# Optimization experiments

Hardware: AMD Instinct MI355X
Metric: run time of the kernel (lower is better)

Reference implementation:

```python
import jax, jax.numpy as jnp
import numpy as np

N_NODES = 100000
N_EDGES = 1600000
D = 128
L = 4          # GIN layers
H = 32         # inner MLP hidden width (hard-coded in create_mlp)
BN_EPS = 1e-5


def setup_inputs() -> dict:
    key = jax.random.key(0)
    ks = jax.random.split(key, 8)
    X = jax.random.normal(ks[0], (N_NODES, D), dtype=jnp.float32)
    edge_index = jax.random.randint(ks[1], (2, N_EDGES), 0, N_NODES, dtype=jnp.int64)
    eps = jax.random.normal(ks[2], (L,), dtype=jnp.float32)
    W1 = jax.random.normal(ks[3], (L, H, D), dtype=jnp.float32) * 0.1
    W2 = jax.random.normal(ks[4], (L, H, H), dtype=jnp.float32) * 0.1
    W3 = jax.random.normal(ks[5], (L, D, H), dtype=jnp.float32) * 0.1
    return {
        "X": X, "edge_index": edge_index, "eps": eps,
        "W1": W1, "b1": jnp.zeros((L, H), jnp.float32),
        "g1": jnp.ones((L, H), jnp.float32), "bt1": jnp.zeros((L, H), jnp.float32),
        "W2": W2, "b2": jnp.zeros((L, H), jnp.float32),
        "g2": jnp.ones((L, H), jnp.float32), "bt2": jnp.zeros((L, H), jnp.float32),
        "W3": W3, "b3": jnp.zeros((L, D), jnp.float32),
    }


def _bn(x, g, b):
    # BatchNorm1d in training mode: biased batch stats over the node axis
    m = jnp.mean(x, axis=0)
    v = jnp.var(x, axis=0)
    return g * (x - m) * jax.lax.rsqrt(v + BN_EPS) + b


def reference(X, edge_index, eps, W1, b1, g1, bt1, W2, b2, g2, bt2, W3, b3):
    src, dst = edge_index[0], edge_index[1]
    for l in range(L):
        # identity-message scatter-add neighbor aggregation
        S = jax.ops.segment_sum(X[src], dst, num_segments=N_NODES)  # [N, D_l]
        Z = (1.0 + eps[l]) * X + S
        # inner MLP: Lin->BN->ReLU, Lin->BN->ReLU, Lin
        h = jax.nn.relu(_bn(Z @ W1[l].T + b1[l], g1[l], bt1[l]))
        h = jax.nn.relu(_bn(h @ W2[l].T + b2[l], g2[l], bt2[l]))
        X = h @ W3[l].T + b3[l]
    return X
```

## Files before the change

kernel.cpp:

```cpp
#include <hip/hip_runtime.h>

#define NN 100000
#define NE 1600000
#define DD 128
#define HH 32
#define NB 196
#define SB 256
#define EPB 6250
#define BCAP 12288
#define QS 25000

#define OFF_P        0UL
#define OFF_T        12800000UL
#define OFF_PK       25600000UL
#define OFF_QOFF     32000000UL
#define OFF_COUNTS   33600128UL
#define OFF_POFS     33800832UL
#define OFF_BTOT     34001536UL
#define OFF_BBASE    34002560UL
#define OFF_STATS    34003584UL
#define OFF_W1T      34019968UL
#define OFF_W2T      34036352UL
#define OFF_MT       34052736UL
#define OFF_C        34065024UL
#define OFF_W3T      34065536UL

__device__ __forceinline__ int src_quad(int s) {
    return (s >= 2 * QS) ? ((s >= 3 * QS) ? 3 : 2) : ((s >= QS) ? 1 : 0);
}

__global__ void __launch_bounds__(256) k_init(const int* __restrict__ ei,
                                              int* __restrict__ counts,
                                              const float* __restrict__ W1,
                                              const float* __restrict__ W2,
                                              const float* __restrict__ W3,
                                              const float* __restrict__ b3,
                                              float* __restrict__ W1T,
                                              float* __restrict__ W2T,
                                              float* __restrict__ MT,
                                              float* __restrict__ C,
                                              float* __restrict__ W3T) {
    int t = threadIdx.x;
    if (blockIdx.x < SB) {
        __shared__ int c[NB];
        if (t < NB) c[t] = 0;
        __syncthreads();
        int s = blockIdx.x * EPB;
        for (int e = s + t; e < s + EPB; e += 256)
            atomicAdd(&c[ei[NE + e] >> 9], 1);
        __syncthreads();
        if (t < NB) counts[t * SB + blockIdx.x] = c[t];
        return;
    }
    int b = blockIdx.x - SB;
    if (b < 12) {
        int d = b * 256 + t;
        int l = d >> 10, rem = d & 1023;
        int i = rem >> 5, j = rem & 31;
        const float* w1r = W1 + (l + 1) * HH * DD + i * DD;
        const float* w3c = W3 + l * DD * HH + j;
        float m = 0.f;
#pragma unroll 8
        for (int k = 0; k < DD; k++) m += w1r[k] * w3c[k * HH];
        MT[l * 1024 + j * 32 + i] = m;
    } else if (b == 12) {
        for (int idx = t; idx < 4096; idx += 256) {
            int jj = idx >> 7, kk = idx & 127;
            W1T[kk * 32 + jj] = W1[jj * 128 + kk];
        }
    } else if (b == 13) {
        for (int idx = t; idx < 4096; idx += 256) {
            int l = idx >> 10, rem = idx & 1023;
            int i = rem >> 5, j = rem & 31;
            W2T[l * 1024 + j * 32 + i] = W2[l * 1024 + i * 32 + j];
        }
    } else if (b == 14) {
        for (int idx = t; idx < 4096; idx += 256) {
            int jj = idx >> 5, kk = idx & 31;
            W3T[kk * 128 + jj] = W3[3 * 4096 + jj * 32 + kk];
        }
    } else {
        if (t < 96) {
            int l = t >> 5, ii = t & 31;
            const float* w1r = W1 + (l + 1) * HH * DD + ii * DD;
            const float* bb = b3 + l * DD;
            float c = 0.f;
#pragma unroll 8
            for (int k = 0; k < DD; k++) c += w1r[k] * bb[k];
            C[l * 32 + ii] = c;
        }
    }
}

__global__ void __launch_bounds__(256) k_scanX(const int* __restrict__ counts,
                                               int* __restrict__ pofs,
                                               int* __restrict__ btot) {
    __shared__ int s[256];
    int t = threadIdx.x, b = blockIdx.x;
    int v = counts[b * SB + t];
    s[t] = v;
    __syncthreads();
    for (int off = 1; off < 256; off <<= 1) {
        int x = (t >= off) ? s[t - off] : 0;
        __syncthreads();
        s[t] += x;
        __syncthreads();
    }
    pofs[b * SB + t] = s[t] - v;
    if (t == 255) btot[b] = s[255];
}

__global__ void __launch_bounds__(256) k_scanY(const int* __restrict__ btot,
                                               int* __restrict__ bbase,
                                               int* __restrict__ qoff) {
    __shared__ int s[256];
    int t = threadIdx.x;
    int v = (t < NB) ? btot[t] : 0;
    s[t] = v;
    __syncthreads();
    for (int off = 1; off < 256; off <<= 1) {
        int x = (t >= off) ? s[t - off] : 0;
        __syncthreads();
        s[t] += x;
        __syncthreads();
    }
    if (t < NB) bbase[t] = s[t] - v;
    if (t == NB - 1) bbase[NB] = s[t];
    if (t == 0) qoff[4 * NN] = NE;
}

__global__ void __launch_bounds__(256) k_scatter(const int* __restrict__ ei,
                                                 const int* __restrict__ pofs,
                                                 const int* __restrict__ bbase,
                                                 int* __restrict__ pk) {
    __shared__ int cur[NB];
    int t = threadIdx.x, blk = blockIdx.x;
    if (t < NB) cur[t] = bbase[t] + pofs[t * SB + blk];
    __syncthreads();
    int s = blk * EPB;
    for (int e = s + t; e < s + EPB; e += 256) {
        int src = ei[e], dst = ei[NE + e];
        int b = dst >> 9;
        int pos = atomicAdd(&cur[b], 1);
        pk[pos] = (src << 9) | (dst & 511);
    }
}

__global__ void __launch_bounds__(256) k_bucket(int* pk,
                                                const int* __restrict__ bbase,
                                                int* __restrict__ qoff) {
    __shared__ int cnt[2048];
    __shared__ int ts[256];
    __shared__ int stage[BCAP];
    int t = threadIdx.x, b = blockIdx.x;
    int base = bbase[b], end = bbase[b + 1];
#pragma unroll
    for (int j = 0; j < 8; j++) cnt[t * 8 + j] = 0;
    __syncthreads();
    for (int e = base + t; e < end; e += 256) {
        int v = pk[e];
        atomicAdd(&cnt[((v & 511) << 2) | src_quad(v >> 9)], 1);
    }
    __syncthreads();
    int c8[8];
    int p = 0;
#pragma unroll
    for (int j = 0; j < 8; j++) { c8[j] = cnt[t * 8 + j]; p += c8[j]; }
    ts[t] = p;
    __syncthreads();
    for (int off = 1; off < 256; off <<= 1) {
        int x = (t >= off) ? ts[t - off] : 0;
        __syncthreads();
        ts[t] += x;
        __syncthreads();
    }
    int run = ts[t] - p;
#pragma unroll
    for (int j = 0; j < 8; j++) {
        int ci = t * 8 + j;
        cnt[ci] = run;
        int n0 = b * 512 + (ci >> 2);
        if (n0 < NN) qoff[n0 * 4 + (ci & 3)] = base + run;
        run += c8[j];
    }
    __syncthreads();
    for (int e = base + t; e < end; e += 256) {
        int v = pk[e];
        int src = v >> 9;
        int pos = atomicAdd(&cnt[((v & 511) << 2) | src_quad(src)], 1);
        stage[pos] = src;
    }
    __syncthreads();
    int sz = end - base;
    for (int i = t; i < sz; i += 256) pk[base + i] = stage[i];
}

__global__ void __launch_bounds__(256) k_P(const float4* __restrict__ X4,
                                           const float4* __restrict__ W1T4,
                                           float4* __restrict__ P4) {
    __shared__ float xs[128 * 33];
    int t = threadIdx.x, blk = blockIdx.x;
    int i = t & 7, g = t >> 3;
    int nbase = blk * 128;
    float4 acc[4];
#pragma unroll
    for (int j = 0; j < 4; j++) acc[j] = make_float4(0.f, 0.f, 0.f, 0.f);
    for (int kt = 0; kt < 4; kt++) {
        __syncthreads();
#pragma unroll
        for (int q = 0; q < 4; q++) {
            int idx = t + 256 * q;
            int nd = idx >> 3, c4 = idx & 7;
            int node = nbase + nd;
            if (node > NN - 1) node = NN - 1;
            float4 v = X4[(size_t)node * 32 + kt * 8 + c4];
            float* dst = xs + nd * 33 + 4 * c4;
            dst[0] = v.x; dst[1] = v.y; dst[2] = v.z; dst[3] = v.w;
        }
        __syncthreads();
        const float4* Wk = W1T4 + (size_t)(kt * 32) * 8 + i;
        const float* xr0 = xs + (g * 4) * 33;
#pragma unroll
        for (int k = 0; k < 32; k++) {
            float4 w = Wk[k * 8];
            float x0 = xr0[k], x1 = xr0[33 + k], x2 = xr0[66 + k], x3 = xr0[99 + k];
            acc[0].x += x0 * w.x; acc[0].y += x0 * w.y; acc[0].z += x0 * w.z; acc[0].w += x0 * w.w;
            acc[1].x += x1 * w.x; acc[1].y += x1 * w.y; acc[1].z += x1 * w.z; acc[1].w += x1 * w.w;
            acc[2].x += x2 * w.x; acc[2].y += x2 * w.y; acc[2].z += x2 * w.z; acc[2].w += x2 * w.w;
            acc[3].x += x3 * w.x; acc[3].y += x3 * w.y; acc[3].z += x3 * w.z; acc[3].w += x3 * w.w;
        }
    }
    int node = nbase + g * 4;
#pragma unroll
    for (int j = 0; j < 4; j++)
        if (node + j < NN) P4[(size_t)(node + j) * 8 + i] = acc[j];
}

__global__ void __launch_bounds__(256) k_A(const float4* __restrict__ P4,
                                           const int* __restrict__ csr,
                                           const int* __restrict__ qoff,
                                           const float* __restrict__ eps,
                                           const float* __restrict__ b1, int l,
                                           float4* __restrict__ T4,
                                           float* __restrict__ gs) {
    __shared__ float ls[64];
    int t = threadIdx.x;
    if (t < 64) ls[t] = 0.f;
    __syncthreads();
    int g = t >> 3, i = t & 7;
    int n = blockIdx.x * 32 + g;
    float e1 = 1.f + eps[l];
    int e0 = qoff[4 * n], eend = qoff[4 * n + 4];
    float4 p = P4[(size_t)n * 8 + i];
    float4 acc;
    acc.x = e1 * p.x; acc.y = e1 * p.y; acc.z = e1 * p.z; acc.w = e1 * p.w;
    int e = e0;
    for (; e + 8 <= eend; e += 8) {
        int s0 = csr[e], s1 = csr[e + 1], s2 = csr[e + 2], s3 = csr[e + 3];
        int s4 = csr[e + 4], s5 = csr[e + 5], s6 = csr[e + 6], s7 = csr[e + 7];
        float4 q0 = P4[(size_t)s0 * 8 + i];
        float4 q1 = P4[(size_t)s1 * 8 + i];
        float4 q2 = P4[(size_t)s2 * 8 + i];
        float4 q3 = P4[(size_t)s3 * 8 + i];
        float4 q4 = P4[(size_t)s4 * 8 + i];
        float4 q5 = P4[(size_t)s5 * 8 + i];
        float4 q6 = P4[(size_t)s6 * 8 + i];
        float4 q7 = P4[(size_t)s7 * 8 + i];
        acc.x += ((q0.x + q1.x) + (q2.x + q3.x)) + ((q4.x + q5.x) + (q6.x + q7.x));
        acc.y += ((q0.y + q1.y) + (q2.y + q3.y)) + ((q4.y + q5.y) + (q6.y + q7.y));
        acc.z += ((q0.z + q1.z) + (q2.z + q3.z)) + ((q4.z + q5.z) + (q6.z + q7.z));
        acc.w += ((q0.w + q1.w) + (q2.w + q3.w)) + ((q4.w + q5.w) + (q6.w + q7.w));
    }
    for (; e + 4 <= eend; e += 4) {
        int s0 = csr[e], s1 = csr[e + 1], s2 = csr[e + 2], s3 = csr[e + 3];
        float4 q0 = P4[(size_t)s0 * 8 + i];
        float4 q1 = P4[(size_t)s1 * 8 + i];
        float4 q2 = P4[(size_t)s2 * 8 + i];
        float4 q3 = P4[(size_t)s3 * 8 + i];
        acc.x += (q0.x + q1.x) + (q2.x + q3.x);
        acc.y += (q0.y + q1.y) + (q2.y + q3.y);
        acc.z += (q0.z + q1.z) + (q2.z + q3.z);
        acc.w += (q0.w + q1.w) + (q2.w + q3.w);
    }
    for (; e < eend; e++) {
        int s = csr[e];
        float4 q = P4[(size_t)s * 8 + i];
        acc.x += q.x; acc.y += q.y; acc.z += q.z; acc.w += q.w;
    }
    float4 bb = ((const float4*)(b1 + l * 32))[i];
    acc.x += bb.x; acc.y += bb.y; acc.z += bb.z; acc.w += bb.w;
    T4[(size_t)n * 8 + i] = acc;
    float sx = acc.x, sy = acc.y, sz = acc.z, sw = acc.w;
    float qx = acc.x * acc.x, qy = acc.y * acc.y, qz = acc.z * acc.z, qw = acc.w * acc.w;
#pragma unroll
    for (int off = 8; off < 64; off <<= 1) {
        sx += __shfl_xor(sx, off); sy += __shfl_xor(sy, off);
        sz += __shfl_xor(sz, off); sw += __shfl_xor(sw, off);
        qx += __shfl_xor(qx, off); qy += __shfl_xor(qy, off);
        qz += __shfl_xor(qz, off); qw += __shfl_xor(qw, off);
    }
    if ((t & 56) == 0) {
        atomicAdd(&ls[4 * i + 0], sx); atomicAdd(&ls[4 * i + 1], sy);
        atomicAdd(&ls[4 * i + 2], sz); atomicAdd(&ls[4 * i + 3], sw);
        atomicAdd(&ls[32 + 4 * i + 0], qx); atomicAdd(&ls[32 + 4 * i + 1], qy);
        atomicAdd(&ls[32 + 4 * i + 2], qz); atomicAdd(&ls[32 + 4 * i + 3], qw);
    }
    __syncthreads();
    if (t < 64) atomicAdd(&gs[(blockIdx.x & 7) * 64 + t], ls[t]);
}

__global__ void __launch_bounds__(256) k_D(float4* __restrict__ T4,
                                           const float4* __restrict__ W2T4,
                                           const float* __restrict__ b2,
                                           const float* __restrict__ g1,
                                           const float* __restrict__ bt1, int l,
                                           float* __restrict__ gs) {
    __shared__ float sc[32], sh[32], ls[64], a1s[128 * 33];
    int t = threadIdx.x, blk = blockIdx.x;
    if (t < 32) {
        float s0 = 0.f, s1 = 0.f;
#pragma unroll
        for (int r = 0; r < 8; r++) { s0 += gs[r * 64 + t]; s1 += gs[r * 64 + 32 + t]; }
        float m = s0 * (1.f / NN);
        float var = s1 * (1.f / NN) - m * m;
        float s = g1[l * 32 + t] * rsqrtf(var + 1e-5f);
        sc[t] = s; sh[t] = bt1[l * 32 + t] - m * s;
    } else if (t >= 64 && t < 128) {
        ls[t - 64] = 0.f;
    }
    __syncthreads();
    int nbase = blk * 128;
#pragma unroll
    for (int q = 0; q < 4; q++) {
        int idx = t + 256 * q;
        int nd = idx >> 3, c4 = idx & 7;
        int node = nbase + nd;
        if (node > NN - 1) node = NN - 1;
        float4 x = T4[(size_t)node * 8 + c4];
        float* dst = a1s + nd * 33 + 4 * c4;
        dst[0] = fmaxf(x.x * sc[4 * c4 + 0] + sh[4 * c4 + 0], 0.f);
        dst[1] = fmaxf(x.y * sc[4 * c4 + 1] + sh[4 * c4 + 1], 0.f);
        dst[2] = fmaxf(x.z * sc[4 * c4 + 2] + sh[4 * c4 + 2], 0.f);
        dst[3] = fmaxf(x.w * sc[4 * c4 + 3] + sh[4 * c4 + 3], 0.f);
    }
    __syncthreads();
    int i = t & 7, g = t >> 3;
    const float4* b24 = (const float4*)(b2 + l * 32);
    float4 b = b24[i];
    float4 acc[4];
#pragma unroll
    for (int j = 0; j < 4; j++) acc[j] = b;
    const float* xr0 = a1s + (g * 4) * 33;
#pragma unroll
    for (int k = 0; k < 32; k++) {
        float4 w = W2T4[k * 8 + i];
        float x0 = xr0[k], x1 = xr0[33 + k], x2 = xr0[66 + k], x3 = xr0[99 + k];
        acc[0].x += x0 * w.x; acc[0].y += x0 * w.y; acc[0].z += x0 * w.z; acc[0].w += x0 * w.w;
        acc[1].x += x1 * w.x; acc[1].y += x1 * w.y; acc[1].z += x1 * w.z; acc[1].w += x1 * w.w;
        acc[2].x += x2 * w.x; acc[2].y += x2 * w.y; acc[2].z += x2 * w.z; acc[2].w += x2 * w.w;
        acc[3].x += x3 * w.x; acc[3].y += x3 * w.y; acc[3].z += x3 * w.z; acc[3].w += x3 * w.w;
    }
    int node = nbase + g * 4;
    float sx = 0.f, sy = 0.f, sz = 0.f, sw = 0.f;
    float qx = 0.f, qy = 0.f, qz = 0.f, qw = 0.f;
#pragma unroll
    for (int j = 0; j < 4; j++) {
        if (node + j < NN) {
            T4[(size_t)(node + j) * 8 + i] = acc[j];
            sx += acc[j].x; sy += acc[j].y; sz += acc[j].z; sw += acc[j].w;
            qx += acc[j].x * acc[j].x; qy += acc[j].y * acc[j].y;
            qz += acc[j].z * acc[j].z; qw += acc[j].w * acc[j].w;
        }
    }
#pragma unroll
    for (int off = 8; off < 64; off <<= 1) {
        sx += __shfl_xor(sx, off); sy += __shfl_xor(sy, off);
        sz += __shfl_xor(sz, off); sw += __shfl_xor(sw, off);
        qx += __shfl_xor(qx, off); qy += __shfl_xor(qy, off);
        qz += __shfl_xor(qz, off); qw += __shfl_xor(qw, off);
    }
    if ((t & 56) == 0) {
        atomicAdd(&ls[4 * i + 0], sx); atomicAdd(&ls[4 * i + 1], sy);
        atomicAdd(&ls[4 * i + 2], sz); atomicAdd(&ls[4 * i + 3], sw);
        atomicAdd(&ls[32 + 4 * i + 0], qx); atomicAdd(&ls[32 + 4 * i + 1], qy);
        atomicAdd(&ls[32 + 4 * i + 2], qz); atomicAdd(&ls[32 + 4 * i + 3], qw);
    }
    __syncthreads();
    if (t < 64) atomicAdd(&gs[512 + (blk & 7) * 64 + t], ls[t]);
}

__global__ void __launch_bounds__(256) k_Fm(const float4* __restrict__ T4,
                                            const float* __restrict__ g2,
                                            const float* __restrict__ bt2, int l,
                                            const float* __restrict__ gs,
                                            const float4* __restrict__ MT4,
                                            const float* __restrict__ C,
                                            float4* __restrict__ P4) {
    __shared__ float sc[32], sh[32], a2s[128 * 33];
    int t = threadIdx.x, blk = blockIdx.x;
    if (t < 32) {
        float s0 = 0.f, s1 = 0.f;
#pragma unroll
        for (int r = 0; r < 8; r++) { s0 += gs[512 + r * 64 + t]; s1 += gs[512 + r * 64 + 32 + t]; }
        float m = s0 * (1.f / NN);
        float var = s1 * (1.f / NN) - m * m;
        float s = g2[l * 32 + t] * rsqrtf(var + 1e-5f);
        sc[t] = s; sh[t] = bt2[l * 32 + t] - m * s;
    }
    __syncthreads();
    int nbase = blk * 128;
#pragma unroll
    for (int q = 0; q < 4; q++) {
        int idx = t + 256 * q;
        int nd = idx >> 3, c4 = idx & 7;
        int node = nbase + nd;
        if (node > NN - 1) node = NN - 1;
        float4 x = T4[(size_t)node * 8 + c4];
        float* dst = a2s + nd * 33 + 4 * c4;
        dst[0] = fmaxf(x.x * sc[4 * c4 + 0] + sh[4 * c4 + 0], 0.f);
        dst[1] = fmaxf(x.y * sc[4 * c4 + 1] + sh[4 * c4 + 1], 0.f);
        dst[2] = fmaxf(x.z * sc[4 * c4 + 2] + sh[4 * c4 + 2], 0.f);
        dst[3] = fmaxf(x.w * sc[4 * c4 + 3] + sh[4 * c4 + 3], 0.f);
    }
    __syncthreads();
    int i = t & 7, g = t >> 3;
    const float4* C4 = (const float4*)(C + l * 32);
    float4 c0 = C4[i];
    float4 acc[4];
#pragma unroll
    for (int j = 0; j < 4; j++) acc[j] = c0;
    const float* xr0 = a2s + (g * 4) * 33;
    const float4* Mt = MT4 + l * 256;
#pragma unroll
    for (int k = 0; k < 32; k++) {
        float4 w = Mt[k * 8 + i];
        float x0 = xr0[k], x1 = xr0[33 + k], x2 = xr0[66 + k], x3 = xr0[99 + k];
        acc[0].x += x0 * w.x; acc[0].y += x0 * w.y; acc[0].z += x0 * w.z; acc[0].w += x0 * w.w;
        acc[1].x += x1 * w.x; acc[1].y += x1 * w.y; acc[1].z += x1 * w.z; acc[1].w += x1 * w.w;
        acc[2].x += x2 * w.x; acc[2].y += x2 * w.y; acc[2].z += x2 * w.z; acc[2].w += x2 * w.w;
        acc[3].x += x3 * w.x; acc[3].y += x3 * w.y; acc[3].z += x3 * w.z; acc[3].w += x3 * w.w;
    }
    int node = nbase + g * 4;
#pragma unroll
    for (int j = 0; j < 4; j++)
        if (node + j < NN) P4[(size_t)(node + j) * 8 + i] = acc[j];
}

__global__ void __launch_bounds__(256) k_F3(const float4* __restrict__ T4,
                                            const float* __restrict__ g2,
                                            const float* __restrict__ bt2,
                                            const float* __restrict__ gs,
                                            const float4* __restrict__ W3T4,
                                            const float* __restrict__ b3,
                                            float4* __restrict__ out4) {
    __shared__ float sc[32], sh[32], a2s[32 * 33];
    int t = threadIdx.x, blk = blockIdx.x;
    if (t < 32) {
        float s0 = 0.f, s1 = 0.f;
#pragma unroll
        for (int r = 0; r < 8; r++) { s0 += gs[512 + r * 64 + t]; s1 += gs[512 + r * 64 + 32 + t]; }
        float m = s0 * (1.f / NN);
        float var = s1 * (1.f / NN) - m * m;
        float s = g2[3 * 32 + t] * rsqrtf(var + 1e-5f);
        sc[t] = s; sh[t] = bt2[3 * 32 + t] - m * s;
    }
    __syncthreads();
    {
        int nd = t >> 3, c4 = t & 7;
        float4 x = T4[(size_t)(blk * 32 + nd) * 8 + c4];
        float* dst = a2s + nd * 33 + 4 * c4;
        dst[0] = fmaxf(x.x * sc[4 * c4 + 0] + sh[4 * c4 + 0], 0.f);
        dst[1] = fmaxf(x.y * sc[4 * c4 + 1] + sh[4 * c4 + 1], 0.f);
        dst[2] = fmaxf(x.z * sc[4 * c4 + 2] + sh[4 * c4 + 2], 0.f);
        dst[3] = fmaxf(x.w * sc[4 * c4 + 3] + sh[4 * c4 + 3], 0.f);
    }
    __syncthreads();
    int j = t & 31, g = t >> 5;
    const float4* b34 = (const float4*)(b3 + 3 * 128);
    float4 b = b34[j];
    float4 acc[4];
#pragma unroll
    for (int jj = 0; jj < 4; jj++) acc[jj] = b;
    const float* xr0 = a2s + (g * 4) * 33;
#pragma unroll
    for (int k = 0; k < 32; k++) {
        float4 w = W3T4[k * 32 + j];
        float x0 = xr0[k], x1 = xr0[33 + k], x2 = xr0[66 + k], x3 = xr0[99 + k];
        acc[0].x += x0 * w.x; acc[0].y += x0 * w.y; acc[0].z += x0 * w.z; acc[0].w += x0 * w.w;
        acc[1].x += x1 * w.x; acc[1].y += x1 * w.y; acc[1].z += x1 * w.z; acc[1].w += x1 * w.w;
        acc[2].x += x2 * w.x; acc[2].y += x2 * w.y; acc[2].z += x2 * w.z; acc[2].w += x2 * w.w;
        acc[3].x += x3 * w.x; acc[3].y += x3 * w.y; acc[3].z += x3 * w.z; acc[3].w += x3 * w.w;
    }
    size_t node = (size_t)blk * 32 + g * 4;
#pragma unroll
    for (int jj = 0; jj < 4; jj++)
        out4[(node + jj) * 32 + j] = acc[jj];
}

extern "C" void kernel_launch(void* const* d_in, const int* in_sizes, int n_in,
                              void* d_out, int out_size, void* d_ws, size_t ws_size,
                              hipStream_t stream) {
    const float* X   = (const float*)d_in[0];
    const int*   EI  = (const int*)d_in[1];
    const float* eps = (const float*)d_in[2];
    const float* W1  = (const float*)d_in[3];
    const float* b1  = (const float*)d_in[4];
    const float* g1  = (const float*)d_in[5];
    const float* bt1 = (const float*)d_in[6];
    const float* W2  = (const float*)d_in[7];
    const float* b2  = (const float*)d_in[8];
    const float* g2  = (const float*)d_in[9];
    const float* bt2 = (const float*)d_in[10];
    const float* W3  = (const float*)d_in[11];
    const float* b3  = (const float*)d_in[12];

    char* ws = (char*)d_ws;
    float* P       = (float*)(ws + OFF_P);
    float* T       = (float*)(ws + OFF_T);
    int*   pk      = (int*)(ws + OFF_PK);
    int*   qoff    = (int*)(ws + OFF_QOFF);
    int*   counts  = (int*)(ws + OFF_COUNTS);
    int*   pofs    = (int*)(ws + OFF_POFS);
    int*   btot    = (int*)(ws + OFF_BTOT);
    int*   bbase   = (int*)(ws + OFF_BBASE);
    float* stats   = (float*)(ws + OFF_STATS);
    float* W1T     = (float*)(ws + OFF_W1T);
    float* W2T     = (float*)(ws + OFF_W2T);
    float* MT      = (float*)(ws + OFF_MT);
    float* C       = (float*)(ws + OFF_C);
    float* W3T     = (float*)(ws + OFF_W3T);

    hipMemsetAsync(ws + OFF_STATS, 0, 16384, stream);

    k_init<<<SB + 16, 256, 0, stream>>>(EI, counts, W1, W2, W3, b3,
                                        W1T, W2T, MT, C, W3T);
    k_scanX<<<NB, 256, 0, stream>>>(counts, pofs, btot);
    k_scanY<<<1, 256, 0, stream>>>(btot, bbase, qoff);
    k_scatter<<<SB, 256, 0, stream>>>(EI, pofs, bbase, pk);
    k_bucket<<<NB, 256, 0, stream>>>(pk, bbase, qoff);
    k_P<<<782, 256, 0, stream>>>((const float4*)X, (const float4*)W1T, (float4*)P);

    for (int l = 0; l < 4; l++) {
        float* gs = stats + l * 1024;
        k_A<<<NN / 32, 256, 0, stream>>>((const float4*)P, pk, qoff, eps, b1, l,
                                         (float4*)T, gs);
        k_D<<<782, 256, 0, stream>>>((float4*)T,
                                     (const float4*)(W2T + (size_t)l * 1024),
                                     b2, g1, bt1, l, gs);
        if (l < 3)
            k_Fm<<<782, 256, 0, stream>>>((const float4*)T, g2, bt2, l, gs,
                                          (const float4*)MT, C, (float4*)P);
        else
            k_F3<<<3125, 256, 0, stream>>>((const float4*)T, g2, bt2, gs,
                                           (const float4*)W3T, b3, (float4*)d_out);
    }
}
```

Before: 462.8 us.

## Fuse preprocessing kernels: fold scans into scatter/bucket, merge P projection into init

Removes the two prefix-scan kernels and the stats memset by having each scatter and bucket block redundantly recompute bucket totals and offsets from the counts matrix. The first-layer projection (k_P) moves into the init launch as extra blocks, each transposing W1 into shared memory instead of reading a precomputed global W1T. The aim is fewer launches and dependency bubbles, at the cost of redundant per-block scans over 196x256 counts and larger shared memory in the init kernel.

```diff
diff --git a/kernel.cpp b/kernel.cpp
--- a/kernel.cpp
+++ b/kernel.cpp
@@ -15,11 +15,7 @@
 #define OFF_PK       25600000UL
 #define OFF_QOFF     32000000UL
 #define OFF_COUNTS   33600128UL
-#define OFF_POFS     33800832UL
-#define OFF_BTOT     34001536UL
-#define OFF_BBASE    34002560UL
 #define OFF_STATS    34003584UL
-#define OFF_W1T      34019968UL
 #define OFF_W2T      34036352UL
 #define OFF_MT       34052736UL
 #define OFF_C        34065024UL
@@ -35,21 +31,24 @@
                                               const float* __restrict__ W2,
                                               const float* __restrict__ W3,
                                               const float* __restrict__ b3,
-                                              float* __restrict__ W1T,
                                               float* __restrict__ W2T,
                                               float* __restrict__ MT,
                                               float* __restrict__ C,
-                                              float* __restrict__ W3T) {
+                                              float* __restrict__ W3T,
+                                              float* __restrict__ stats,
+                                              const float4* __restrict__ X4,
+                                              float4* __restrict__ P4) {
+    __shared__ __align__(16) char smem[33280];
     int t = threadIdx.x;
     if (blockIdx.x < SB) {
-        __shared__ int c[NB];
+        int* c = (int*)smem;
         if (t < NB) c[t] = 0;
         __syncthreads();
         int s = blockIdx.x * EPB;
         for (int e = s + t; e < s + EPB; e += 256)
             atomicAdd(&c[ei[NE + e] >> 9], 1);
         __syncthreads();
-        if (t < NB) counts[t * SB + blockIdx.x] = c[t];
+        if (t < NB) counts[blockIdx.x * 256 + t] = c[t];
         return;
     }
     int b = blockIdx.x - SB;
@@ -63,23 +62,21 @@
 #pragma unroll 8
         for (int k = 0; k < DD; k++) m += w1r[k] * w3c[k * HH];
         MT[l * 1024 + j * 32 + i] = m;
+        return;
     } else if (b == 12) {
-        for (int idx = t; idx < 4096; idx += 256) {
-            int jj = idx >> 7, kk = idx & 127;
-            W1T[kk * 32 + jj] = W1[jj * 128 + kk];
-        }
-    } else if (b == 13) {
         for (int idx = t; idx < 4096; idx += 256) {
             int l = idx >> 10, rem = idx & 1023;
             int i = rem >> 5, j = rem & 31;
             W2T[l * 1024 + j * 32 + i] = W2[l * 1024 + i * 32 + j];
         }
-    } else if (b == 14) {
+        return;
+    } else if (b == 13) {
         for (int idx = t; idx < 4096; idx += 256) {
             int jj = idx >> 5, kk = idx & 31;
             W3T[kk * 128 + jj] = W3[3 * 4096 + jj * 32 + kk];
         }
-    } else {
+        return;
+    } else if (b == 14) {
         if (t < 96) {
             int l = t >> 5, ii = t & 31;
             const float* w1r = W1 + (l + 1) * HH * DD + ii * DD;
@@ -89,117 +86,17 @@
             for (int k = 0; k < DD; k++) c += w1r[k] * bb[k];
             C[l * 32 + ii] = c;
         }
-    }
-}
-
-__global__ void __launch_bounds__(256) k_scanX(const int* __restrict__ counts,
-                                               int* __restrict__ pofs,
-                                               int* __restrict__ btot) {
-    __shared__ int s[256];
-    int t = threadIdx.x, b = blockIdx.x;
-    int v = counts[b * SB + t];
-    s[t] = v;
-    __syncthreads();
-    for (int off = 1; off < 256; off <<= 1) {
-        int x = (t >= off) ? s[t - off] : 0;
-        __syncthreads();
-        s[t] += x;
-        __syncthreads();
-    }
-    pofs[b * SB + t] = s[t] - v;
-    if (t == 255) btot[b] = s[255];
-}
-
-__global__ void __launch_bounds__(256) k_scanY(const int* __restrict__ btot,
-                                               int* __restrict__ bbase,
-                                               int* __restrict__ qoff) {
-    __shared__ int s[256];
-    int t = threadIdx.x;
-    int v = (t < NB) ? btot[t] : 0;
-    s[t] = v;
-    __syncthreads();
-    for (int off = 1; off < 256; off <<= 1) {
-        int x = (t >= off) ? s[t - off] : 0;
-        __syncthreads();
-        s[t] += x;
-        __syncthreads();
-    }
-    if (t < NB) bbase[t] = s[t] - v;
-    if (t == NB - 1) bbase[NB] = s[t];
-    if (t == 0) qoff[4 * NN] = NE;
-}
-
-__global__ void __launch_bounds__(256) k_scatter(const int* __restrict__ ei,
-                                                 const int* __restrict__ pofs,
-                                                 const int* __restrict__ bbase,
-                                                 int* __restrict__ pk) {
-    __shared__ int cur[NB];
-    int t = threadIdx.x, blk = blockIdx.x;
-    if (t < NB) cur[t] = bbase[t] + pofs[t * SB + blk];
-    __syncthreads();
-    int s = blk * EPB;
-    for (int e = s + t; e < s + EPB; e += 256) {
-        int src = ei[e], dst = ei[NE + e];
-        int b = dst >> 9;
-        int pos = atomicAdd(&cur[b], 1);
-        pk[pos] = (src << 9) | (dst & 511);
-    }
-}
-
-__global__ void __launch_bounds__(256) k_bucket(int* pk,
-                                                const int* __restrict__ bbase,
-                                                int* __restrict__ qoff) {
-    __shared__ int cnt[2048];
-    __shared__ int ts[256];
-    __shared__ int stage[BCAP];
-    int t = threadIdx.x, b = blockIdx.x;
-    int base = bbase[b], end = bbase[b + 1];
-#pragma unroll
-    for (int j = 0; j < 8; j++) cnt[t * 8 + j] = 0;
-    __syncthreads();
-    for (int e = base + t; e < end; e += 256) {
-        int v = pk[e];
-        atomicAdd(&cnt[((v & 511) << 2) | src_quad(v >> 9)], 1);
-    }
-    __syncthreads();
-    int c8[8];
-    int p = 0;
-#pragma unroll
-    for (int j = 0; j < 8; j++) { c8[j] = cnt[t * 8 + j]; p += c8[j]; }
-    ts[t] = p;
-    __syncthreads();
-    for (int off = 1; off < 256; off <<= 1) {
-        int x = (t >= off) ? ts[t - off] : 0;
-        __syncthreads();
-        ts[t] += x;
-        __syncthreads();
-    }
-    int run = ts[t] - p;
-#pragma unroll
-    for (int j = 0; j < 8; j++) {
-        int ci = t * 8 + j;
-        cnt[ci] = run;
-        int n0 = b * 512 + (ci >> 2);
-        if (n0 < NN) qoff[n0 * 4 + (ci & 3)] = base + run;
-        run += c8[j];
-    }
-    __syncthreads();
-    for (int e = base + t; e < end; e += 256) {
-        int v = pk[e];
-        int src = v >> 9;
-        int pos = atomicAdd(&cnt[((v & 511) << 2) | src_quad(src)], 1);
-        stage[pos] = src;
-    }
-    __syncthreads();
-    int sz = end - base;
-    for (int i = t; i < sz; i += 256) pk[base + i] = stage[i];
-}
-
-__global__ void __launch_bounds__(256) k_P(const float4* __restrict__ X4,
-                                           const float4* __restrict__ W1T4,
-                                           float4* __restrict__ P4) {
-    __shared__ float xs[128 * 33];
-    int t = threadIdx.x, blk = blockIdx.x;
+        for (int idx = t; idx < 4096; idx += 256) stats[idx] = 0.f;
+        return;
+    }
+    int blk = b - 15;
+    float* xs = (float*)smem;
+    float* ws = (float*)(smem + 16896);
+    for (int d = t; d < 4096; d += 256) {
+        int kk = d >> 5, jj = d & 31;
+        ws[d] = W1[jj * 128 + kk];
+    }
+    const float4* ws4 = (const float4*)ws;
     int i = t & 7, g = t >> 3;
     int nbase = blk * 128;
     float4 acc[4];
@@ -218,7 +115,7 @@
             dst[0] = v.x; dst[1] = v.y; dst[2] = v.z; dst[3] = v.w;
         }
         __syncthreads();
-        const float4* Wk = W1T4 + (size_t)(kt * 32) * 8 + i;
+        const float4* Wk = ws4 + (size_t)(kt * 32) * 8 + i;
         const float* xr0 = xs + (g * 4) * 33;
 #pragma unroll
         for (int k = 0; k < 32; k++) {
@@ -234,6 +131,103 @@
 #pragma unroll
     for (int j = 0; j < 4; j++)
         if (node + j < NN) P4[(size_t)(node + j) * 8 + i] = acc[j];
+}
+
+__global__ void __launch_bounds__(256) k_scatter(const int* __restrict__ ei,
+                                                 const int* __restrict__ counts,
+                                                 int* __restrict__ pk) {
+    __shared__ int ts[256];
+    __shared__ int cur[NB];
+    int t = threadIdx.x, blk = blockIdx.x;
+    int partial = 0, total = 0;
+    if (t < NB) {
+        for (int j = 0; j < SB; j++) {
+            int c = counts[j * 256 + t];
+            total += c;
+            if (j < blk) partial += c;
+        }
+    }
+    ts[t] = (t < NB) ? total : 0;
+    __syncthreads();
+    for (int off = 1; off < 256; off <<= 1) {
+        int x = (t >= off) ? ts[t - off] : 0;
+        __syncthreads();
+        ts[t] += x;
+        __syncthreads();
+    }
+    if (t < NB) cur[t] = (ts[t] - total) + partial;
+    __syncthreads();
+    int s = blk * EPB;
+    for (int e = s + t; e < s + EPB; e += 256) {
+        int src = ei[e], dst = ei[NE + e];
+        int b = dst >> 9;
+        int pos = atomicAdd(&cur[b], 1);
+        pk[pos] = (src << 9) | (dst & 511);
+    }
+}
+
+__global__ void __launch_bounds__(256) k_bucket(int* pk,
+                                                const int* __restrict__ counts,
+                                                int* __restrict__ qoff) {
+    __shared__ int cnt[2048];
+    __shared__ int ts[256];
+    __shared__ int stage[BCAP];
+    int t = threadIdx.x, b = blockIdx.x;
+    int total = 0;
+    if (t < NB) {
+        for (int j = 0; j < SB; j++) total += counts[j * 256 + t];
+    }
+    ts[t] = (t < NB) ? total : 0;
+    __syncthreads();
+    for (int off = 1; off < 256; off <<= 1) {
+        int x = (t >= off) ? ts[t - off] : 0;
+        __syncthreads();
+        ts[t] += x;
+        __syncthreads();
+    }
+    int base = (b == 0) ? 0 : ts[b - 1];
+    int end  = ts[b];
+    if (b == 0 && t == 0) qoff[4 * NN] = NE;
+    __syncthreads();
+#pragma unroll
+    for (int j = 0; j < 8; j++) cnt[t * 8 + j] = 0;
+    __syncthreads();
+    for (int e = base + t; e < end; e += 256) {
+        int v = pk[e];
+        atomicAdd(&cnt[((v & 511) << 2) | src_quad(v >> 9)], 1);
+    }
+    __syncthreads();
+    int c8[8];
+    int p = 0;
+#pragma unroll
+    for (int j = 0; j < 8; j++) { c8[j] = cnt[t * 8 + j]; p += c8[j]; }
+    ts[t] = p;
+    __syncthreads();
+    for (int off = 1; off < 256; off <<= 1) {
+        int x = (t >= off) ? ts[t - off] : 0;
+        __syncthreads();
+        ts[t] += x;
+        __syncthreads();
+    }
+    int run = ts[t] - p;
+#pragma unroll
+    for (int j = 0; j < 8; j++) {
+        int ci = t * 8 + j;
+        cnt[ci] = run;
+        int n0 = b * 512 + (ci >> 2);
+        if (n0 < NN) qoff[n0 * 4 + (ci & 3)] = base + run;
+        run += c8[j];
+    }
+    __syncthreads();
+    for (int e = base + t; e < end; e += 256) {
+        int v = pk[e];
+        int src = v >> 9;
+        int pos = atomicAdd(&cnt[((v & 511) << 2) | src_quad(src)], 1);
+        stage[pos] = src;
+    }
+    __syncthreads();
+    int sz = end - base;
+    for (int i = t; i < sz; i += 256) pk[base + i] = stage[i];
 }
 
 __global__ void __launch_bounds__(256) k_A(const float4* __restrict__ P4,
@@ -520,25 +514,17 @@
     int*   pk      = (int*)(ws + OFF_PK);
     int*   qoff    = (int*)(ws + OFF_QOFF);
     int*   counts  = (int*)(ws + OFF_COUNTS);
-    int*   pofs    = (int*)(ws + OFF_POFS);
-    int*   btot    = (int*)(ws + OFF_BTOT);
-    int*   bbase   = (int*)(ws + OFF_BBASE);
     float* stats   = (float*)(ws + OFF_STATS);
-    float* W1T     = (float*)(ws + OFF_W1T);
     float* W2T     = (float*)(ws + OFF_W2T);
     float* MT      = (float*)(ws + OFF_MT);
     float* C       = (float*)(ws + OFF_C);
     float* W3T     = (float*)(ws + OFF_W3T);
 
-    hipMemsetAsync(ws + OFF_STATS, 0, 16384, stream);
-
-    k_init<<<SB + 16, 256, 0, stream>>>(EI, counts, W1, W2, W3, b3,
-                                        W1T, W2T, MT, C, W3T);
-    k_scanX<<<NB, 256, 0, stream>>>(counts, pofs, btot);
-    k_scanY<<<1, 256, 0, stream>>>(btot, bbase, qoff);
-    k_scatter<<<SB, 256, 0, stream>>>(EI, pofs, bbase, pk);
-    k_bucket<<<NB, 256, 0, stream>>>(pk, bbase, qoff);
-    k_P<<<782, 256, 0, stream>>>((const float4*)X, (const float4*)W1T, (float4*)P);
+    k_init<<<SB + 15 + 782, 256, 0, stream>>>(EI, counts, W1, W2, W3, b3,
+                                              W2T, MT, C, W3T, stats,
+                                              (const float4*)X, (float4*)P);
+    k_scatter<<<SB, 256, 0, stream>>>(EI, counts, pk);
+    k_bucket<<<NB, 256, 0, stream>>>(pk, counts, qoff);
 
     for (int l = 0; l < 4; l++) {
         float* gs = stats + l * 1024;
```

Measured after the change: 478.6 us. 1.03x slower.
